# Kernel optimization log

Hardware: AMD Instinct MI355X
Metric: run time of the kernel (lower is better)

Reference implementation:

```python
import jax, jax.numpy as jnp
import numpy as np

B, A = 4096, 8          # episodes, agents per episode
N = B * A               # total nodes
E = B * A * (A - 1)     # fully-connected directed edges within each group
F_IN, D, H, M, NA = 64, 64, 4, 64, 10  # in_feat, gnn_dim, heads, mem_dim, n_actions
NEG_SLOPE = 0.2
LN_EPS = 1e-5


def _build_edge_index():
    base = np.arange(A)
    s = np.repeat(base, A)
    d = np.tile(base, A)
    keep = s != d
    s, d = s[keep], d[keep]                       # [A*(A-1)]
    offs = (np.arange(B) * A)[:, None]
    src = (offs + s[None, :]).reshape(-1)
    dst = (offs + d[None, :]).reshape(-1)
    return jnp.asarray(np.stack([src, dst]), dtype=jnp.int32)  # [2, E]


def setup_inputs() -> dict:
    key = jax.random.key(0)
    ks = jax.random.split(key, 16)
    sc = 0.05
    return {
        "x": jax.random.normal(ks[0], (N, F_IN), jnp.float32),
        "edge_attr": jax.random.normal(ks[1], (E, 3), jnp.float32),
        "hidden": jax.random.normal(ks[2], (N, M), jnp.float32) * sc,
        "edge_index": _build_edge_index(),
        # GATv2 params
        "Wl": jax.random.normal(ks[3], (H * D, F_IN), jnp.float32) * sc,
        "bl": jnp.zeros((H * D,), jnp.float32),
        "Wr": jax.random.normal(ks[4], (H * D, F_IN), jnp.float32) * sc,
        "br": jnp.zeros((H * D,), jnp.float32),
        "We": jax.random.normal(ks[5], (H * D, 3), jnp.float32) * sc,
        "be": jnp.zeros((H * D,), jnp.float32),
        "att": jax.random.normal(ks[6], (H, D), jnp.float32) * sc,
        "bias_g": jnp.zeros((D,), jnp.float32),
        # GRUCell params (gate order r,z,n as in torch)
        "W_ih": jax.random.normal(ks[7], (3 * M, D), jnp.float32) * sc,
        "W_hh": jax.random.normal(ks[8], (3 * M, M), jnp.float32) * sc,
        "b_ih": jnp.zeros((3 * M,), jnp.float32),
        "b_hh": jnp.zeros((3 * M,), jnp.float32),
        # LayerNorm + output Linear
        "ln_g": jnp.ones((M,), jnp.float32),
        "ln_b": jnp.zeros((M,), jnp.float32),
        "Wq": jax.random.normal(ks[9], (NA, M), jnp.float32) * sc,
        "bq": jnp.zeros((NA,), jnp.float32),
    }


def reference(x, edge_attr, hidden, edge_index, Wl, bl, Wr, br, We, be, att,
              bias_g, W_ih, W_hh, b_ih, b_hh, ln_g, ln_b, Wq, bq):
    src, dst = edge_index[0], edge_index[1]
    # GATv2Conv (concat=False -> mean over heads), share_weights=False
    xl = (x @ Wl.T + bl).reshape(N, H, D)          # source projection
    xr = (x @ Wr.T + br).reshape(N, H, D)          # target projection
    ee = (edge_attr @ We.T + be).reshape(E, H, D)  # edge embedding
    m = jax.nn.leaky_relu(xl[src] + xr[dst] + ee, NEG_SLOPE)  # [E,H,D]
    logits = jnp.einsum('ehd,hd->eh', m, att)                  # [E,H]
    lmax = jax.ops.segment_max(logits, dst, num_segments=N)    # [N,H]
    ex = jnp.exp(logits - lmax[dst])
    denom = jax.ops.segment_sum(ex, dst, num_segments=N)       # [N,H]
    alpha = ex / denom[dst]                                    # softmax per target
    agg = jax.ops.segment_sum(alpha[:, :, None] * xl[src], dst, num_segments=N)  # [N,H,D]
    h_gnn = jax.nn.relu(agg.mean(axis=1) + bias_g)             # [N,D]
    # GRUCell
    gi = h_gnn @ W_ih.T + b_ih
    gh = hidden @ W_hh.T + b_hh
    ir, iz, inn = jnp.split(gi, 3, axis=-1)
    hr, hz, hn = jnp.split(gh, 3, axis=-1)
    r = jax.nn.sigmoid(ir + hr)
    z = jax.nn.sigmoid(iz + hz)
    n = jnp.tanh(inn + r * hn)
    h = (1.0 - z) * n + z * hidden                              # [N,M]
    # LayerNorm + Linear head
    mu = h.mean(axis=-1, keepdims=True)
    var = ((h - mu) ** 2).mean(axis=-1, keepdims=True)
    hln = (h - mu) / jnp.sqrt(var + LN_EPS) * ln_g + ln_b
    q = hln @ Wq.T + bq                                         # [N,NA]
    return q, h
```

## Files before the change

### kernel.cpp

```cpp
#include <hip/hip_runtime.h>

typedef unsigned short u16;
typedef __attribute__((ext_vector_type(8))) short bf16x8;
typedef __attribute__((ext_vector_type(4))) float f32x4;

#define NAG 8
#define NAGB 16
#define FIN 64
#define MDIM 64
#define NACT 10
#define EPG 56
#define NTOT 32768
#define ABP 72
#define XLS 296
#define XHS 72

#define U_XR 4736
#define U_RZ 0
#define U_IN 2048
#define U_HN 3072
#define U_LN 4096

__device__ __forceinline__ float b2f(u16 u) {
  return __uint_as_float(((unsigned int)u) << 16);
}
__device__ __forceinline__ u16 f2b(float f) {
  unsigned int x = __float_as_uint(f);
  unsigned int r = x + 0x7fffu + ((x >> 16) & 1u);
  return (u16)(r >> 16);
}

__global__ __launch_bounds__(256) void prep_weights(
    const float* __restrict__ Wl, const float* __restrict__ Wr,
    const float* __restrict__ Wih, const float* __restrict__ Whh,
    u16* __restrict__ wsB)
{
  const int idx = blockIdx.x * 256 + threadIdx.x;
  if (idx >= 56 * 2 * 64) return;
  const int L  = idx & 63;
  const int ks = (idx >> 6) & 1;
  const int T  = idx >> 7;
  const float* W; int row0;
  if      (T < 16) { W = Wl;  row0 = T * 16; }
  else if (T < 32) { W = Wr;  row0 = (T - 16) * 16; }
  else if (T < 44) { W = Wih; row0 = (T - 32) * 16; }
  else             { W = Whh; row0 = (T - 44) * 16; }
  const int row = row0 + (L & 15);
  const int k0  = ks * 32 + (L >> 4) * 8;
  u16 v[8];
#pragma unroll
  for (int j = 0; j < 8; j++) v[j] = f2b(W[row * 64 + k0 + j]);
  *(bf16x8*)(wsB + (size_t)idx * 8) = *(bf16x8*)v;
}

__global__ __launch_bounds__(256, 4) void gnn_rnn_kernel(
    const float* __restrict__ x, const float* __restrict__ edge_attr,
    const float* __restrict__ hidden,
    const float* __restrict__ bl, const float* __restrict__ br,
    const float* __restrict__ We, const float* __restrict__ be,
    const float* __restrict__ att, const float* __restrict__ bias_g,
    const float* __restrict__ b_ih, const float* __restrict__ b_hh,
    const float* __restrict__ ln_g, const float* __restrict__ ln_b,
    const float* __restrict__ Wq, const float* __restrict__ bq,
    const u16* __restrict__ wsB,
    float* __restrict__ d_out)
{
  __shared__ __align__(16) char uraw[20736];
  __shared__ __align__(16) u16 s_xb[NAGB * ABP];
  __shared__ __align__(16) u16 s_hidb[NAGB * ABP];
  __shared__ __align__(16) u16 s_hgb[NAGB * ABP];
  __shared__ float s_ea[2 * EPG * 3];
  __shared__ __align__(16) u16 s_blb[256], s_brb[256];
  __shared__ __align__(16) u16 s_w0b[288], s_w1b[288], s_w2b[288], s_beb[288], s_attb[288];
  __shared__ float s_alpha[2 * EPG][4];
  __shared__ float s_bih[192], s_bhh[192];

  u16*   uXL = (u16*)uraw;
  u16*   uXR = (u16*)uraw + U_XR;
  float* uF  = (float*)uraw;

  const int t = threadIdx.x;
  const int b = blockIdx.x;
  const int L = t & 63;
  const int w = t >> 6;
  const int q = L >> 4;

  {
    const float* xb = x + b * (NAGB * FIN);
    const float* hb = hidden + b * (NAGB * MDIM);
#pragma unroll
    for (int i = t; i < NAGB * FIN; i += 256) {
      const int a = i >> 6, m = i & 63;
      s_xb[a * ABP + m] = f2b(xb[i]);
      s_hidb[a * ABP + m] = f2b(hb[i]);
    }
    const float* eb = edge_attr + b * (2 * EPG * 3);
    for (int i = t; i < 2 * EPG * 3; i += 256) s_ea[i] = eb[i];
    s_blb[t] = f2b(bl[t]);  s_brb[t] = f2b(br[t]);
    {
      const int h = t >> 6, d = t & 63, idx = h * XHS + d;
      s_beb[idx]  = f2b(be[t]);
      s_attb[idx] = f2b(att[t]);
      s_w0b[idx]  = f2b(We[t * 3]);
      s_w1b[idx]  = f2b(We[t * 3 + 1]);
      s_w2b[idx]  = f2b(We[t * 3 + 2]);
    }
    if (t < 192)  { s_bih[t] = b_ih[t]; s_bhh[t] = b_hh[t]; }
  }
  __syncthreads();

  {
    const int arow = L & 15;
    bf16x8 af0 = *(const bf16x8*)&s_xb[arow * ABP + q * 8];
    bf16x8 af1 = *(const bf16x8*)&s_xb[arow * ABP + 32 + q * 8];
    const bf16x8* wsBv = (const bf16x8*)wsB;
#pragma unroll 4
    for (int i = 0; i < 8; i++) {
      const int T = w * 8 + i;
      f32x4 acc = {0.f, 0.f, 0.f, 0.f};
      acc = __builtin_amdgcn_mfma_f32_16x16x32_bf16(af0, wsBv[(T * 2 + 0) * 64 + L], acc, 0, 0, 0);
      acc = __builtin_amdgcn_mfma_f32_16x16x32_bf16(af1, wsBv[(T * 2 + 1) * 64 + L], acc, 0, 0, 0);
      const int col = L & 15;
      const int Tm = T & 15;
      const int h = Tm >> 2, d = (Tm & 3) * 16 + col;
      const int gc = Tm * 16 + col;
      if (T < 16) {
        const float bias = b2f(s_blb[gc]);
#pragma unroll
        for (int r = 0; r < 4; r++)
          uXL[(q * 4 + r) * XLS + h * XHS + d] = f2b(acc[r] + bias);
      } else {
        const float bias = b2f(s_brb[gc]);
#pragma unroll
        for (int r = 0; r < 4; r++)
          uXR[(q * 4 + r) * XLS + h * XHS + d] = f2b(acc[r] + bias);
      }
    }
  }
  __syncthreads();

  for (int ep = 0; ep < 2; ep++) {
    if (t < EPG * 4) {
      const int e = t % 56, h = t / 56;
      const int s = e / 7, k = e % 7;
      const int j = k + (k >= s ? 1 : 0);
      const int eg = ep * EPG + e;
      const float ea0 = s_ea[eg * 3], ea1 = s_ea[eg * 3 + 1], ea2 = s_ea[eg * 3 + 2];
      const u16* xlp = uXL + (ep * 8 + s) * XLS + h * XHS;
      const u16* xrp = uXR + (ep * 8 + j) * XLS + h * XHS;
      const u16* w0p = s_w0b + h * XHS;
      const u16* w1p = s_w1b + h * XHS;
      const u16* w2p = s_w2b + h * XHS;
      const u16* bep = s_beb + h * XHS;
      const u16* atp = s_attb + h * XHS;
      float lg = 0.f;
#pragma unroll 2
      for (int kq = 0; kq < 8; kq++) {
        bf16x8 vxl = *(const bf16x8*)(xlp + kq * 8);
        bf16x8 vxr = *(const bf16x8*)(xrp + kq * 8);
        bf16x8 v0  = *(const bf16x8*)(w0p + kq * 8);
        bf16x8 v1  = *(const bf16x8*)(w1p + kq * 8);
        bf16x8 v2  = *(const bf16x8*)(w2p + kq * 8);
        bf16x8 vb  = *(const bf16x8*)(bep + kq * 8);
        bf16x8 va  = *(const bf16x8*)(atp + kq * 8);
#pragma unroll
        for (int c = 0; c < 8; c++) {
          float mv = b2f((u16)vxl[c]) + b2f((u16)vxr[c])
                   + ea0 * b2f((u16)v0[c]) + ea1 * b2f((u16)v1[c])
                   + ea2 * b2f((u16)v2[c]) + b2f((u16)vb[c]);
          mv = mv > 0.f ? mv : 0.2f * mv;
          lg += mv * b2f((u16)va[c]);
        }
      }
      s_alpha[eg][h] = lg;
    }
  }
  __syncthreads();

  if (t < 64) {
    const int ep = t >> 5, j = (t >> 2) & 7, h = t & 3;
    const int e0 = ep * EPG;
    float mx = -1e30f;
#pragma unroll
    for (int s = 0; s < 8; s++) {
      if (s == j) continue;
      int e = e0 + s * 7 + (j > s ? j - 1 : j);
      mx = fmaxf(mx, s_alpha[e][h]);
    }
    float sum = 0.f;
#pragma unroll
    for (int s = 0; s < 8; s++) {
      if (s == j) continue;
      int e = e0 + s * 7 + (j > s ? j - 1 : j);
      float ex = __expf(s_alpha[e][h] - mx);
      s_alpha[e][h] = ex;
      sum += ex;
    }
    float inv = 1.f / sum;
#pragma unroll
    for (int s = 0; s < 8; s++) {
      if (s == j) continue;
      int e = e0 + s * 7 + (j > s ? j - 1 : j);
      s_alpha[e][h] *= inv;
    }
  }
  __syncthreads();

  {
    const int ep = t >> 7, jj = (t >> 4) & 7, dq = t & 15;
    const int a16 = ep * 8 + jj;
    float acc[4] = {0.f, 0.f, 0.f, 0.f};
#pragma unroll 2
    for (int h = 0; h < 4; h++) {
#pragma unroll
      for (int s = 0; s < 8; s++) {
        if (s == jj) continue;
        int e = ep * EPG + s * 7 + (jj > s ? jj - 1 : jj);
        float al = s_alpha[e][h];
        const u16* xp = uXL + (ep * 8 + s) * XLS + h * XHS + dq * 4;
        ushort4 xv = *(const ushort4*)xp;
        acc[0] += al * b2f(xv.x);
        acc[1] += al * b2f(xv.y);
        acc[2] += al * b2f(xv.z);
        acc[3] += al * b2f(xv.w);
      }
    }
    const f32x4 bg = *(const f32x4*)(bias_g + dq * 4);
    u16 pk[4];
#pragma unroll
    for (int c = 0; c < 4; c++) {
      float v = acc[c] * 0.25f + bg[c];
      pk[c] = f2b(v > 0.f ? v : 0.f);
    }
    *(uint2*)&s_hgb[a16 * ABP + dq * 4] = *(uint2*)pk;
  }
  __syncthreads();

  {
    const int arow = L & 15;
    bf16x8 ag0 = *(const bf16x8*)&s_hgb[arow * ABP + q * 8];
    bf16x8 ag1 = *(const bf16x8*)&s_hgb[arow * ABP + 32 + q * 8];
    bf16x8 ah0 = *(const bf16x8*)&s_hidb[arow * ABP + q * 8];
    bf16x8 ah1 = *(const bf16x8*)&s_hidb[arow * ABP + 32 + q * 8];
    const bf16x8* wsBv = (const bf16x8*)wsB;
#pragma unroll
    for (int i = 0; i < 3; i++) {
      const int T6 = w * 3 + i;
      const int Tg = 32 + T6, Th = 44 + T6;
      f32x4 acci = {0.f, 0.f, 0.f, 0.f};
      acci = __builtin_amdgcn_mfma_f32_16x16x32_bf16(ag0, wsBv[(Tg * 2 + 0) * 64 + L], acci, 0, 0, 0);
      acci = __builtin_amdgcn_mfma_f32_16x16x32_bf16(ag1, wsBv[(Tg * 2 + 1) * 64 + L], acci, 0, 0, 0);
      f32x4 acch = {0.f, 0.f, 0.f, 0.f};
      acch = __builtin_amdgcn_mfma_f32_16x16x32_bf16(ah0, wsBv[(Th * 2 + 0) * 64 + L], acch, 0, 0, 0);
      acch = __builtin_amdgcn_mfma_f32_16x16x32_bf16(ah1, wsBv[(Th * 2 + 1) * 64 + L], acch, 0, 0, 0);
      const int col = L & 15;
      const int gc = T6 * 16 + col;
      if (T6 < 8) {
#pragma unroll
        for (int r = 0; r < 4; r++)
          uF[U_RZ + (q * 4 + r) * 128 + gc] = acci[r] + acch[r] + s_bih[gc] + s_bhh[gc];
      } else {
#pragma unroll
        for (int r = 0; r < 4; r++) {
          uF[U_IN + (q * 4 + r) * 64 + gc - 128] = acci[r] + s_bih[gc];
          uF[U_HN + (q * 4 + r) * 64 + gc - 128] = acch[r] + s_bhh[gc];
        }
      }
    }
  }
  __syncthreads();

  {
    const float lng = ln_g[L];
    const float lnb = ln_b[L];
#pragma unroll
    for (int rr = 0; rr < 4; rr++) {
      const int a = w + rr * 4, m = L;
      float rz_r = uF[U_RZ + a * 128 + m];
      float rz_z = uF[U_RZ + a * 128 + 64 + m];
      float inn  = uF[U_IN + a * 64 + m];
      float hn   = uF[U_HN + a * 64 + m];
      float hid  = hidden[(b * NAGB + a) * MDIM + m];
      float r = 1.f / (1.f + __expf(-rz_r));
      float z = 1.f / (1.f + __expf(-rz_z));
      float xg = inn + r * hn;
      xg = fminf(fmaxf(xg, -20.f), 20.f);
      float e2 = __expf(2.f * xg);
      float n = (e2 - 1.f) / (e2 + 1.f);
      float hv = (1.f - z) * n + z * hid;
      d_out[NTOT * NACT + (b * NAGB + a) * MDIM + m] = hv;
      float sum = hv;
#pragma unroll
      for (int off = 1; off < 64; off <<= 1) sum += __shfl_xor(sum, off, 64);
      float mu = sum * (1.f / 64.f);
      float dv = hv - mu;
      float s2 = dv * dv;
#pragma unroll
      for (int off = 1; off < 64; off <<= 1) s2 += __shfl_xor(s2, off, 64);
      float var = s2 * (1.f / 64.f);
      uF[U_LN + a * 68 + m] = dv * rsqrtf(var + 1e-5f) * lng + lnb;
    }
  }
  __syncthreads();

  if (t < NAGB * NACT) {
    const int a = t / NACT, o = t % NACT;
    float acc = bq[o];
    const float4* lv = (const float4*)(uF + U_LN + a * 68);
    const float4* wv = (const float4*)(Wq + o * 64);
#pragma unroll 4
    for (int kq = 0; kq < 16; kq++) {
      float4 l4 = lv[kq], w4 = wv[kq];
      acc += l4.x * w4.x + l4.y * w4.y + l4.z * w4.z + l4.w * w4.w;
    }
    d_out[(b * NAGB + a) * NACT + o] = acc;
  }
}

extern "C" void kernel_launch(void* const* d_in, const int* in_sizes, int n_in,
                              void* d_out, int out_size, void* d_ws, size_t ws_size,
                              hipStream_t stream) {
  const int N  = in_sizes[0] / FIN;
  const int Bn = N / NAGB;
  u16* wsB = (u16*)d_ws;

  prep_weights<<<28, 256, 0, stream>>>(
      (const float*)d_in[4],
      (const float*)d_in[6],
      (const float*)d_in[12],
      (const float*)d_in[13],
      wsB);

  gnn_rnn_kernel<<<Bn, 256, 0, stream>>>(
      (const float*)d_in[0], (const float*)d_in[1], (const float*)d_in[2],
      (const float*)d_in[5],
      (const float*)d_in[7],
      (const float*)d_in[8],
      (const float*)d_in[9],
      (const float*)d_in[10],
      (const float*)d_in[11],
      (const float*)d_in[14],
      (const float*)d_in[15],
      (const float*)d_in[16], (const float*)d_in[17],
      (const float*)d_in[18], (const float*)d_in[19],
      wsB, (float*)d_out);
}
```

Measured before the change: 157.3 us.

## Shrink LDS footprint and vectorize GATv2 edge logit math

The bias arrays bl, br, b_ih and b_hh are no longer staged in shared memory and are read straight from global. The GRU input-gate scratch is stored as bf16 in a compacted union region, which lowers per-block LDS so more blocks can be resident. The edge-logit loop is rewritten with float4 vector arithmetic and a max-based leaky ReLU. Storing inn in bf16 adds rounding error to the GRU candidate gate.

```diff
diff --git a/kernel.cpp b/kernel.cpp
--- a/kernel.cpp
+++ b/kernel.cpp
@@ -15,11 +15,11 @@
 #define XLS 296
 #define XHS 72
 
-#define U_XR 4736
-#define U_RZ 0
-#define U_IN 2048
-#define U_HN 3072
-#define U_LN 4096
+#define U_XR  4736
+#define U_RZ  0
+#define U_HN  2048
+#define U_LN  3072
+#define U_INB 8320
 
 __device__ __forceinline__ float b2f(u16 u) {
   return __uint_as_float(((unsigned int)u) << 16);
@@ -28,6 +28,10 @@
   unsigned int x = __float_as_uint(f);
   unsigned int r = x + 0x7fffu + ((x >> 16) & 1u);
   return (u16)(r >> 16);
+}
+__device__ __forceinline__ void b8tov(bf16x8 v, f32x4& lo, f32x4& hi) {
+#pragma unroll
+  for (int c = 0; c < 4; c++) { lo[c] = b2f((u16)v[c]); hi[c] = b2f((u16)v[c + 4]); }
 }
 
 __global__ __launch_bounds__(256) void prep_weights(
@@ -65,19 +69,18 @@
     const u16* __restrict__ wsB,
     float* __restrict__ d_out)
 {
-  __shared__ __align__(16) char uraw[20736];
+  __shared__ __align__(16) char uraw[18944];
   __shared__ __align__(16) u16 s_xb[NAGB * ABP];
   __shared__ __align__(16) u16 s_hidb[NAGB * ABP];
   __shared__ __align__(16) u16 s_hgb[NAGB * ABP];
   __shared__ float s_ea[2 * EPG * 3];
-  __shared__ __align__(16) u16 s_blb[256], s_brb[256];
   __shared__ __align__(16) u16 s_w0b[288], s_w1b[288], s_w2b[288], s_beb[288], s_attb[288];
   __shared__ float s_alpha[2 * EPG][4];
-  __shared__ float s_bih[192], s_bhh[192];
-
-  u16*   uXL = (u16*)uraw;
-  u16*   uXR = (u16*)uraw + U_XR;
-  float* uF  = (float*)uraw;
+
+  u16*   uXL  = (u16*)uraw;
+  u16*   uXR  = (u16*)uraw + U_XR;
+  u16*   uInn = (u16*)uraw + U_INB;
+  float* uF   = (float*)uraw;
 
   const int t = threadIdx.x;
   const int b = blockIdx.x;
@@ -96,7 +99,6 @@
     }
     const float* eb = edge_attr + b * (2 * EPG * 3);
     for (int i = t; i < 2 * EPG * 3; i += 256) s_ea[i] = eb[i];
-    s_blb[t] = f2b(bl[t]);  s_brb[t] = f2b(br[t]);
     {
       const int h = t >> 6, d = t & 63, idx = h * XHS + d;
       s_beb[idx]  = f2b(be[t]);
@@ -105,7 +107,6 @@
       s_w1b[idx]  = f2b(We[t * 3 + 1]);
       s_w2b[idx]  = f2b(We[t * 3 + 2]);
     }
-    if (t < 192)  { s_bih[t] = b_ih[t]; s_bhh[t] = b_hh[t]; }
   }
   __syncthreads();
 
@@ -125,12 +126,12 @@
       const int h = Tm >> 2, d = (Tm & 3) * 16 + col;
       const int gc = Tm * 16 + col;
       if (T < 16) {
-        const float bias = b2f(s_blb[gc]);
+        const float bias = bl[gc];
 #pragma unroll
         for (int r = 0; r < 4; r++)
           uXL[(q * 4 + r) * XLS + h * XHS + d] = f2b(acc[r] + bias);
       } else {
-        const float bias = b2f(s_brb[gc]);
+        const float bias = br[gc];
 #pragma unroll
         for (int r = 0; r < 4; r++)
           uXR[(q * 4 + r) * XLS + h * XHS + d] = f2b(acc[r] + bias);
@@ -153,26 +154,27 @@
       const u16* w2p = s_w2b + h * XHS;
       const u16* bep = s_beb + h * XHS;
       const u16* atp = s_attb + h * XHS;
-      float lg = 0.f;
+      f32x4 lgv = {0.f, 0.f, 0.f, 0.f};
 #pragma unroll 2
       for (int kq = 0; kq < 8; kq++) {
-        bf16x8 vxl = *(const bf16x8*)(xlp + kq * 8);
-        bf16x8 vxr = *(const bf16x8*)(xrp + kq * 8);
-        bf16x8 v0  = *(const bf16x8*)(w0p + kq * 8);
-        bf16x8 v1  = *(const bf16x8*)(w1p + kq * 8);
-        bf16x8 v2  = *(const bf16x8*)(w2p + kq * 8);
-        bf16x8 vb  = *(const bf16x8*)(bep + kq * 8);
-        bf16x8 va  = *(const bf16x8*)(atp + kq * 8);
-#pragma unroll
-        for (int c = 0; c < 8; c++) {
-          float mv = b2f((u16)vxl[c]) + b2f((u16)vxr[c])
-                   + ea0 * b2f((u16)v0[c]) + ea1 * b2f((u16)v1[c])
-                   + ea2 * b2f((u16)v2[c]) + b2f((u16)vb[c]);
-          mv = mv > 0.f ? mv : 0.2f * mv;
-          lg += mv * b2f((u16)va[c]);
+        f32x4 xlL, xlH, xrL, xrH, w0L, w0H, w1L, w1H, w2L, w2H, bbL, bbH, atL, atH;
+        b8tov(*(const bf16x8*)(xlp + kq * 8), xlL, xlH);
+        b8tov(*(const bf16x8*)(xrp + kq * 8), xrL, xrH);
+        b8tov(*(const bf16x8*)(w0p + kq * 8), w0L, w0H);
+        b8tov(*(const bf16x8*)(w1p + kq * 8), w1L, w1H);
+        b8tov(*(const bf16x8*)(w2p + kq * 8), w2L, w2H);
+        b8tov(*(const bf16x8*)(bep + kq * 8), bbL, bbH);
+        b8tov(*(const bf16x8*)(atp + kq * 8), atL, atH);
+        f32x4 mL = xlL + xrL + bbL + w0L * ea0 + w1L * ea1 + w2L * ea2;
+        f32x4 mH = xlH + xrH + bbH + w0H * ea0 + w1H * ea1 + w2H * ea2;
+#pragma unroll
+        for (int c = 0; c < 4; c++) {
+          mL[c] = fmaxf(mL[c], 0.2f * mL[c]);
+          mH[c] = fmaxf(mH[c], 0.2f * mH[c]);
         }
+        lgv += mL * atL + mH * atH;
       }
-      s_alpha[eg][h] = lg;
+      s_alpha[eg][h] = lgv[0] + lgv[1] + lgv[2] + lgv[3];
     }
   }
   __syncthreads();
@@ -256,14 +258,16 @@
       const int col = L & 15;
       const int gc = T6 * 16 + col;
       if (T6 < 8) {
+        const float bsum = b_ih[gc] + b_hh[gc];
 #pragma unroll
         for (int r = 0; r < 4; r++)
-          uF[U_RZ + (q * 4 + r) * 128 + gc] = acci[r] + acch[r] + s_bih[gc] + s_bhh[gc];
+          uF[U_RZ + (q * 4 + r) * 128 + gc] = acci[r] + acch[r] + bsum;
       } else {
+        const float bi = b_ih[gc], bh = b_hh[gc];
 #pragma unroll
         for (int r = 0; r < 4; r++) {
-          uF[U_IN + (q * 4 + r) * 64 + gc - 128] = acci[r] + s_bih[gc];
-          uF[U_HN + (q * 4 + r) * 64 + gc - 128] = acch[r] + s_bhh[gc];
+          uInn[(q * 4 + r) * 64 + gc - 128] = f2b(acci[r] + bi);
+          uF[U_HN + (q * 4 + r) * 64 + gc - 128] = acch[r] + bh;
         }
       }
     }
@@ -278,7 +282,7 @@
       const int a = w + rr * 4, m = L;
       float rz_r = uF[U_RZ + a * 128 + m];
       float rz_z = uF[U_RZ + a * 128 + 64 + m];
-      float inn  = uF[U_IN + a * 64 + m];
+      float inn  = b2f(uInn[a * 64 + m]);
       float hn   = uF[U_HN + a * 64 + m];
       float hid  = hidden[(b * NAGB + a) * MDIM + m];
       float r = 1.f / (1.f + __expf(-rz_r));
```

New measurement: 154.1 us. 1.02x faster.
